# Kernel optimization log

Measured on AMD Instinct MI355X. Metric: run time of the kernel, lower is better.

The kernel has to match this reference:

```python
import jax, jax.numpy as jnp
import numpy as np

N = 50000      # nodes
E = 800000     # edges (avg degree 16)
DIN = 128
H = 128
DOUT = 64


def setup_inputs() -> dict:
    key = jax.random.key(0)
    ks = jax.random.split(key, 8)
    x = jax.random.normal(ks[0], (N, DIN), dtype=jnp.float32)
    edge_index = jax.random.randint(ks[1], (2, E), 0, N, dtype=jnp.int32)
    def glorot(k, fi, fo):
        return jax.random.normal(k, (fi, fo), dtype=jnp.float32) * (1.0 / np.sqrt(fi))
    return {
        "x": x,
        "edge_index": edge_index,
        "W1": glorot(ks[2], DIN, H), "b1": jnp.zeros((H,), jnp.float32),
        "W2": glorot(ks[3], H, H),   "b2": jnp.zeros((H,), jnp.float32),
        "W3": glorot(ks[4], H, DOUT),"b3": jnp.zeros((DOUT,), jnp.float32),
    }


def reference(x, edge_index, W1, b1, W2, b2, W3, b3):
    n = x.shape[0]
    # GCNConv: add self-loops, symmetric degree normalization D^-1/2 (A+I) D^-1/2
    loop = jnp.arange(n, dtype=edge_index.dtype)
    src = jnp.concatenate([edge_index[0], loop])  # [E+N]
    dst = jnp.concatenate([edge_index[1], loop])
    deg = jax.ops.segment_sum(jnp.ones(src.shape, x.dtype), dst, num_segments=n)
    dinv = jnp.where(deg > 0, jax.lax.rsqrt(deg), 0.0)
    norm = dinv[src] * dinv[dst]  # [E+N]

    def conv(h, W, b):
        h = h @ W                                   # [N, out]
        msg = h[src] * norm[:, None]                # gather + scale
        return jax.ops.segment_sum(msg, dst, num_segments=n) + b

    # gelu after every layer except the last (forward breaks before act)
    h = jax.nn.gelu(conv(x, W1, b1), approximate=False)
    h = jax.nn.gelu(conv(h, W2, b2), approximate=False)
    return conv(h, W3, b3)
```

## Files before the change

kernel.cpp:

```cpp
#include <hip/hip_runtime.h>
#include <math.h>

#define NDIN 128
#define NHID 128
#define NDOUT 64

typedef _Float16 half2_t __attribute__((ext_vector_type(2)));
typedef _Float16 half4_t __attribute__((ext_vector_type(4)));
typedef _Float16 half8_t __attribute__((ext_vector_type(8)));
typedef float    float4v __attribute__((ext_vector_type(4)));

__device__ __forceinline__ float gelu_exact(float x) {
    return 0.5f * x * (1.0f + erff(x * 0.70710678118654752f));
}


__global__ void count_kernel(const int* __restrict__ dst, int* __restrict__ count, int E) {
    int e = blockIdx.x * blockDim.x + threadIdx.x;
    if (e < E) atomicAdd(&count[dst[e]], 1);
}

__global__ __launch_bounds__(256) void reduce_blocks_kernel(
    const int* __restrict__ count, int* __restrict__ blocksum, int n) {
    __shared__ int s[256];
    int i = blockIdx.x * 256 + threadIdx.x;
    s[threadIdx.x] = (i < n) ? count[i] : 0;
    __syncthreads();
    for (int off = 128; off > 0; off >>= 1) {
        if (threadIdx.x < off) s[threadIdx.x] += s[threadIdx.x + off];
        __syncthreads();
    }
    if (threadIdx.x == 0) blocksum[blockIdx.x] = s[0];
}

__global__ __launch_bounds__(256) void scan_partials_kernel(
    const int* __restrict__ blocksum, int* __restrict__ blockoff,
    int* __restrict__ rowptr, int nb, int n) {
    __shared__ int s[256];
    int t = threadIdx.x;
    int v = (t < nb) ? blocksum[t] : 0;
    s[t] = v;
    __syncthreads();
    for (int off = 1; off < 256; off <<= 1) {
        int u = (t >= off) ? s[t - off] : 0;
        __syncthreads();
        s[t] += u;
        __syncthreads();
    }
    if (t < nb) blockoff[t] = s[t] - v;
    if (t == 255) rowptr[n] = s[255];
}

__global__ __launch_bounds__(256) void scan_blocks_kernel(
    const int* __restrict__ count, const int* __restrict__ blockoff,
    int* __restrict__ rowptr, float* __restrict__ dinv, int n) {
    __shared__ int s[256];
    int i = blockIdx.x * 256 + threadIdx.x;
    int v = (i < n) ? count[i] : 0;
    s[threadIdx.x] = v;
    __syncthreads();
    for (int off = 1; off < 256; off <<= 1) {
        int u = (threadIdx.x >= off) ? s[threadIdx.x - off] : 0;
        __syncthreads();
        s[threadIdx.x] += u;
        __syncthreads();
    }
    if (i < n) {
        rowptr[i] = blockoff[blockIdx.x] + s[threadIdx.x] - v;
        dinv[i] = rsqrtf((float)(v + 1));
    }
}

__global__ void fill_kernel(const int* __restrict__ src, const int* __restrict__ dst,
                            const float* __restrict__ dinv, const int* __restrict__ rowptr,
                            int* __restrict__ count, int2* __restrict__ adj, int E) {
    int e = blockIdx.x * blockDim.x + threadIdx.x;
    if (e >= E) return;
    int s = src[e], d = dst[e];
    int slot = atomicSub(&count[d], 1) - 1;
    int p = rowptr[d] + slot;
    adj[p] = make_int2(s, __float_as_int(dinv[s] * dinv[d]));
}

__global__ __launch_bounds__(256) void wtrans_kernel(
    const float* __restrict__ W, _Float16* __restrict__ Wt, int K, int N) {
    __shared__ float tile[32][33];
    int tx = threadIdx.x & 31, ty = threadIdx.x >> 5;
    for (int i = 0; i < 32; i += 8) {
        int k = blockIdx.y * 32 + ty + i, n = blockIdx.x * 32 + tx;
        tile[ty + i][tx] = (k < K && n < N) ? W[(size_t)k * N + n] : 0.f;
    }
    __syncthreads();
    for (int i = 0; i < 32; i += 8) {
        int n = blockIdx.x * 32 + ty + i, k = blockIdx.y * 32 + tx;
        if (n < N && k < K) Wt[(size_t)n * K + k] = (_Float16)tile[tx][ty + i];
    }
}


template <int BN, bool AF16>
__global__ __launch_bounds__(256) void gemm_mfma(
    const void* __restrict__ Aptr, const _Float16* __restrict__ Bt,
    _Float16* __restrict__ T, int M) {
    __shared__ _Float16 lds_a[64][136];
    __shared__ _Float16 lds_bt[BN][136];
    const int K = 128;
    int tid = threadIdx.x;
    int bm = blockIdx.x * 64;
    int wave = tid >> 6, lane = tid & 63;
    int m = lane & 15, quad = lane >> 4;

    if (AF16) {
        const _Float16* A = (const _Float16*)Aptr;
#pragma unroll
        for (int j = 0; j < 4; j++) {
            int c = tid + j * 256;
            int r = c >> 4, col = (c & 15) << 3;
            int grow = bm + r;
            uint4 v = make_uint4(0, 0, 0, 0);
            if (grow < M) v = *(const uint4*)(A + (size_t)grow * K + col);
            *(uint4*)&lds_a[r][col] = v;
        }
    } else {
        const float* A = (const float*)Aptr;
#pragma unroll
        for (int j = 0; j < 8; j++) {
            int c = tid + j * 256;
            int r = c >> 5, col = (c & 31) << 2;
            int grow = bm + r;
            float4 v = make_float4(0.f, 0.f, 0.f, 0.f);
            if (grow < M) v = *(const float4*)(A + (size_t)grow * K + col);
            half4_t h;
            h[0] = (_Float16)v.x; h[1] = (_Float16)v.y;
            h[2] = (_Float16)v.z; h[3] = (_Float16)v.w;
            *(half4_t*)&lds_a[r][col] = h;
        }
    }
    {
        const int chunks = BN * K / 8;
        for (int c = tid; c < chunks; c += 256) {
            int r = c >> 4, col = (c & 15) << 3;
            *(uint4*)&lds_bt[r][col] = *(const uint4*)(Bt + (size_t)r * K + col);
        }
    }
    __syncthreads();

    const int NT = BN / 16;
    float4v acc[NT];
#pragma unroll
    for (int nt = 0; nt < NT; nt++) acc[nt] = (float4v){0.f, 0.f, 0.f, 0.f};

    int arow = (wave << 4) + m;
#pragma unroll
    for (int kc = 0; kc < K; kc += 32) {
        half8_t a = *(const half8_t*)&lds_a[arow][kc + quad * 8];
#pragma unroll
        for (int nt = 0; nt < NT; nt++) {
            half8_t b = *(const half8_t*)&lds_bt[nt * 16 + m][kc + quad * 8];
            acc[nt] = __builtin_amdgcn_mfma_f32_16x16x32_f16(a, b, acc[nt], 0, 0, 0);
        }
    }
#pragma unroll
    for (int nt = 0; nt < NT; nt++) {
#pragma unroll
        for (int r = 0; r < 4; r++) {
            int grow = bm + (wave << 4) + (quad << 2) + r;
            if (grow < M) T[(size_t)grow * BN + nt * 16 + m] = (_Float16)acc[nt][r];
        }
    }
}


template <int F, bool DOGELU, bool OUTF16>
__global__ __launch_bounds__(256) void agg_kernel(
    const _Float16* __restrict__ t, const int* __restrict__ rowptr,
    const int2* __restrict__ adj, const float* __restrict__ dinv,
    const float* __restrict__ bias, void* __restrict__ outp, int n) {
    int node = (int)((blockIdx.x * blockDim.x + threadIdx.x) >> 6);
    int lane = threadIdx.x & 63;
    if (node >= n) return;

    float wself = dinv[node];
    wself *= wself;
    int beg = rowptr[node];
    int end = rowptr[node + 1];

    if (F == 128) {
        const half2_t* t2 = (const half2_t*)t;
        half2_t v = t2[(size_t)node * 64 + lane];
        float accx = wself * (float)v[0], accy = wself * (float)v[1];
        for (int e0 = beg; e0 < end; e0 += 64) {
            int rem = end - e0;
            int j = 0; float w = 0.f;
            if (lane < rem) {
                int2 ed = adj[e0 + lane];
                j = ed.x; w = __int_as_float(ed.y);
            }
            int cnt = rem < 64 ? rem : 64;
            for (int c = 0; c < cnt; c += 16) {
#pragma unroll
                for (int i = 0; i < 16; i++) {
                    int jj = __builtin_amdgcn_readlane(j, c + i);
                    float ww = __int_as_float(
                        __builtin_amdgcn_readlane(__float_as_int(w), c + i));
                    half2_t u = t2[(size_t)jj * 64 + lane];
                    accx += ww * (float)u[0];
                    accy += ww * (float)u[1];
                }
            }
        }
        float2 b = ((const float2*)bias)[lane];
        accx += b.x; accy += b.y;
        if (DOGELU) { accx = gelu_exact(accx); accy = gelu_exact(accy); }
        if (OUTF16) {
            half2_t o; o[0] = (_Float16)accx; o[1] = (_Float16)accy;
            ((half2_t*)outp)[(size_t)node * 64 + lane] = o;
        } else {
            float2 o; o.x = accx; o.y = accy;
            ((float2*)outp)[(size_t)node * 64 + lane] = o;
        }
    } else {
        float acc = wself * (float)t[(size_t)node * 64 + lane];
        for (int e0 = beg; e0 < end; e0 += 64) {
            int rem = end - e0;
            int j = 0; float w = 0.f;
            if (lane < rem) {
                int2 ed = adj[e0 + lane];
                j = ed.x; w = __int_as_float(ed.y);
            }
            int cnt = rem < 64 ? rem : 64;
            for (int c = 0; c < cnt; c += 16) {
#pragma unroll
                for (int i = 0; i < 16; i++) {
                    int jj = __builtin_amdgcn_readlane(j, c + i);
                    float ww = __int_as_float(
                        __builtin_amdgcn_readlane(__float_as_int(w), c + i));
                    acc += ww * (float)t[(size_t)jj * 64 + lane];
                }
            }
        }
        acc += bias[lane];
        if (DOGELU) acc = gelu_exact(acc);
        if (OUTF16) ((_Float16*)outp)[(size_t)node * 64 + lane] = (_Float16)acc;
        else        ((float*)outp)[(size_t)node * 64 + lane] = acc;
    }
}


extern "C" void kernel_launch(void* const* d_in, const int* in_sizes, int n_in,
                              void* d_out, int out_size, void* d_ws, size_t ws_size,
                              hipStream_t stream) {
    const float* x  = (const float*)d_in[0];
    const int* edge = (const int*)d_in[1];
    const float* W1 = (const float*)d_in[2];
    const float* b1 = (const float*)d_in[3];
    const float* W2 = (const float*)d_in[4];
    const float* b2 = (const float*)d_in[5];
    const float* W3 = (const float*)d_in[6];
    const float* b3 = (const float*)d_in[7];
    float* out = (float*)d_out;

    const int N = in_sizes[0] / NDIN;
    const int E = in_sizes[1] / 2;
    const int* src = edge;
    const int* dst = edge + E;
    const int NB = (N + 255) / 256;

    char* p = (char*)d_ws;
    auto alloc = [&](size_t bytes) {
        char* q = p;
        p += (bytes + 255) & ~(size_t)255;
        return q;
    };
    int*       count    = (int*)alloc((size_t)N * 4);
    int*       rowptr   = (int*)alloc((size_t)(N + 1) * 4);
    int*       blocksum = (int*)alloc((size_t)NB * 4);
    int*       blockoff = (int*)alloc((size_t)NB * 4);
    float*     dinv     = (float*)alloc((size_t)N * 4);
    int2*      adj      = (int2*)alloc((size_t)E * 8);
    _Float16*  W1t      = (_Float16*)alloc((size_t)NHID * NDIN * 2);
    _Float16*  W2t      = (_Float16*)alloc((size_t)NHID * NHID * 2);
    _Float16*  W3t      = (_Float16*)alloc((size_t)NDOUT * NHID * 2);
    _Float16*  tbuf     = (_Float16*)alloc((size_t)N * NHID * 2);
    _Float16*  hbuf     = (_Float16*)alloc((size_t)N * NHID * 2);

    hipMemsetAsync(count, 0, (size_t)N * 4, stream);

    count_kernel<<<(E + 255) / 256, 256, 0, stream>>>(dst, count, E);
    reduce_blocks_kernel<<<NB, 256, 0, stream>>>(count, blocksum, N);
    scan_partials_kernel<<<1, 256, 0, stream>>>(blocksum, blockoff, rowptr, NB, N);
    scan_blocks_kernel<<<NB, 256, 0, stream>>>(count, blockoff, rowptr, dinv, N);
    fill_kernel<<<(E + 255) / 256, 256, 0, stream>>>(src, dst, dinv, rowptr, count,
                                                     adj, E);
    wtrans_kernel<<<dim3(NHID / 32, NDIN / 32), 256, 0, stream>>>(W1, W1t, NDIN, NHID);
    wtrans_kernel<<<dim3(NHID / 32, NHID / 32), 256, 0, stream>>>(W2, W2t, NHID, NHID);
    wtrans_kernel<<<dim3(NDOUT / 32, NHID / 32), 256, 0, stream>>>(W3, W3t, NHID, NDOUT);

    dim3 blk(256);
    int mtiles = (N + 63) / 64;
    int agg_blocks = (N + 3) / 4;

    gemm_mfma<128, false><<<mtiles, blk, 0, stream>>>(x, W1t, tbuf, N);
    agg_kernel<128, true, true><<<agg_blocks, blk, 0, stream>>>(tbuf, rowptr, adj,
                                                                dinv, b1, hbuf, N);
    gemm_mfma<128, true><<<mtiles, blk, 0, stream>>>(hbuf, W2t, tbuf, N);
    agg_kernel<128, true, true><<<agg_blocks, blk, 0, stream>>>(tbuf, rowptr, adj,
                                                                dinv, b2, hbuf, N);
    gemm_mfma<64, true><<<mtiles, blk, 0, stream>>>(hbuf, W3t, tbuf, N);
    agg_kernel<64, false, false><<<agg_blocks, blk, 0, stream>>>(tbuf, rowptr, adj,
                                                                 dinv, b3, out, N);
}
```

Measured before the change: 292.7 us.

## Merge preprocessing launches and vectorize aggregation with 16-byte gathers

Folds the memset and three weight transposes into one prep kernel. The block reduce and partial scan become a single kernel using a last-block-done atomic, and the edge fill is co-launched with the first GEMM. The aggregation kernel now has lane groups each handle a different neighbor with 8-wide half loads, followed by a cross-group shuffle reduction. The goal is to cut launch overhead and issue fewer, wider gather loads, at the cost of extra shuffle reductions and idle lanes during the epilogue.

```diff
diff --git a/kernel.cpp b/kernel.cpp
--- a/kernel.cpp
+++ b/kernel.cpp
@@ -15,30 +15,71 @@
 }
 
 
+__device__ void wtrans_tile(const float* __restrict__ W, _Float16* __restrict__ Wt,
+                            int K, int N, int bx, int by) {
+    __shared__ float tile[32][33];
+    int tx = threadIdx.x & 31, ty = threadIdx.x >> 5;
+    for (int i = 0; i < 32; i += 8) {
+        int k = by * 32 + ty + i, nn = bx * 32 + tx;
+        tile[ty + i][tx] = (k < K && nn < N) ? W[(size_t)k * N + nn] : 0.f;
+    }
+    __syncthreads();
+    for (int i = 0; i < 32; i += 8) {
+        int nn = bx * 32 + ty + i, k = by * 32 + tx;
+        if (nn < N && k < K) Wt[(size_t)nn * K + k] = (_Float16)tile[tx][ty + i];
+    }
+}
+
+__global__ __launch_bounds__(256) void prep0_kernel(
+    const float* __restrict__ W1, _Float16* __restrict__ W1t,
+    const float* __restrict__ W2, _Float16* __restrict__ W2t,
+    const float* __restrict__ W3, _Float16* __restrict__ W3t,
+    int* __restrict__ count, int* __restrict__ done, int n) {
+    int b = blockIdx.x;
+    if (b < 16) {
+        wtrans_tile(W1, W1t, NDIN, NHID, b & 3, b >> 2);
+    } else if (b < 32) {
+        wtrans_tile(W2, W2t, NHID, NHID, (b - 16) & 3, (b - 16) >> 2);
+    } else if (b < 40) {
+        wtrans_tile(W3, W3t, NHID, NDOUT, (b - 32) & 1, (b - 32) >> 1);
+    } else {
+        int z = b - 40;
+        int i = z * 256 + threadIdx.x;
+        if (i < n) count[i] = 0;
+        if (z == 0 && threadIdx.x == 0) *done = 0;
+    }
+}
+
+
 __global__ void count_kernel(const int* __restrict__ dst, int* __restrict__ count, int E) {
     int e = blockIdx.x * blockDim.x + threadIdx.x;
     if (e < E) atomicAdd(&count[dst[e]], 1);
 }
 
-__global__ __launch_bounds__(256) void reduce_blocks_kernel(
-    const int* __restrict__ count, int* __restrict__ blocksum, int n) {
+
+__global__ __launch_bounds__(256) void reduce_scanp_kernel(
+    const int* __restrict__ count, int* __restrict__ blocksum, int* __restrict__ blockoff,
+    int* __restrict__ rowptr, int* __restrict__ done, int nb, int n) {
     __shared__ int s[256];
-    int i = blockIdx.x * 256 + threadIdx.x;
-    s[threadIdx.x] = (i < n) ? count[i] : 0;
+    __shared__ int islast;
+    int t = threadIdx.x;
+    int i = blockIdx.x * 256 + t;
+    s[t] = (i < n) ? count[i] : 0;
     __syncthreads();
     for (int off = 128; off > 0; off >>= 1) {
-        if (threadIdx.x < off) s[threadIdx.x] += s[threadIdx.x + off];
-        __syncthreads();
-    }
-    if (threadIdx.x == 0) blocksum[blockIdx.x] = s[0];
-}
-
-__global__ __launch_bounds__(256) void scan_partials_kernel(
-    const int* __restrict__ blocksum, int* __restrict__ blockoff,
-    int* __restrict__ rowptr, int nb, int n) {
-    __shared__ int s[256];
-    int t = threadIdx.x;
-    int v = (t < nb) ? blocksum[t] : 0;
+        if (t < off) s[t] += s[t + off];
+        __syncthreads();
+    }
+    if (t == 0) {
+        atomicExch(&blocksum[blockIdx.x], s[0]);
+        __threadfence();
+        int old = atomicAdd(done, 1);
+        islast = (old == nb - 1) ? 1 : 0;
+    }
+    __syncthreads();
+    if (!islast) return;
+    __threadfence();
+    int v = (t < nb) ? atomicAdd(&blocksum[t], 0) : 0;
     s[t] = v;
     __syncthreads();
     for (int off = 1; off < 256; off <<= 1) {
@@ -50,6 +91,7 @@
     if (t < nb) blockoff[t] = s[t] - v;
     if (t == 255) rowptr[n] = s[255];
 }
+
 
 __global__ __launch_bounds__(256) void scan_blocks_kernel(
     const int* __restrict__ count, const int* __restrict__ blockoff,
@@ -71,42 +113,15 @@
     }
 }
 
-__global__ void fill_kernel(const int* __restrict__ src, const int* __restrict__ dst,
-                            const float* __restrict__ dinv, const int* __restrict__ rowptr,
-                            int* __restrict__ count, int2* __restrict__ adj, int E) {
-    int e = blockIdx.x * blockDim.x + threadIdx.x;
-    if (e >= E) return;
-    int s = src[e], d = dst[e];
-    int slot = atomicSub(&count[d], 1) - 1;
-    int p = rowptr[d] + slot;
-    adj[p] = make_int2(s, __float_as_int(dinv[s] * dinv[d]));
-}
-
-__global__ __launch_bounds__(256) void wtrans_kernel(
-    const float* __restrict__ W, _Float16* __restrict__ Wt, int K, int N) {
-    __shared__ float tile[32][33];
-    int tx = threadIdx.x & 31, ty = threadIdx.x >> 5;
-    for (int i = 0; i < 32; i += 8) {
-        int k = blockIdx.y * 32 + ty + i, n = blockIdx.x * 32 + tx;
-        tile[ty + i][tx] = (k < K && n < N) ? W[(size_t)k * N + n] : 0.f;
-    }
-    __syncthreads();
-    for (int i = 0; i < 32; i += 8) {
-        int n = blockIdx.x * 32 + ty + i, k = blockIdx.y * 32 + tx;
-        if (n < N && k < K) Wt[(size_t)n * K + k] = (_Float16)tile[tx][ty + i];
-    }
-}
-
 
 template <int BN, bool AF16>
-__global__ __launch_bounds__(256) void gemm_mfma(
-    const void* __restrict__ Aptr, const _Float16* __restrict__ Bt,
-    _Float16* __restrict__ T, int M) {
+__device__ void gemm_body(const void* __restrict__ Aptr, const _Float16* __restrict__ Bt,
+                          _Float16* __restrict__ T, int M, int blk) {
     __shared__ _Float16 lds_a[64][136];
     __shared__ _Float16 lds_bt[BN][136];
     const int K = 128;
     int tid = threadIdx.x;
-    int bm = blockIdx.x * 64;
+    int bm = blk * 64;
     int wave = tid >> 6, lane = tid & 63;
     int m = lane & 15, quad = lane >> 4;
 
@@ -170,79 +185,107 @@
     }
 }
 
+template <int BN, bool AF16>
+__global__ __launch_bounds__(256) void gemm_mfma(
+    const void* __restrict__ Aptr, const _Float16* __restrict__ Bt,
+    _Float16* __restrict__ T, int M) {
+    gemm_body<BN, AF16>(Aptr, Bt, T, M, blockIdx.x);
+}
+
+
+__global__ __launch_bounds__(256) void fill_gemm1_kernel(
+    const int* __restrict__ src, const int* __restrict__ dst,
+    const float* __restrict__ dinv, const int* __restrict__ rowptr,
+    int* __restrict__ count, int2* __restrict__ adj, int E,
+    const float* __restrict__ x, const _Float16* __restrict__ W1t,
+    _Float16* __restrict__ T, int M, int gemmBlocks) {
+    int b = blockIdx.x;
+    if (b < gemmBlocks) {
+        gemm_body<128, false>(x, W1t, T, M, b);
+        return;
+    }
+    int e = (b - gemmBlocks) * 256 + threadIdx.x;
+    if (e >= E) return;
+    int s = src[e], d = dst[e];
+    int slot = atomicSub(&count[d], 1) - 1;
+    int p = rowptr[d] + slot;
+    adj[p] = make_int2(s, __float_as_int(dinv[s] * dinv[d]));
+}
+
 
 template <int F, bool DOGELU, bool OUTF16>
 __global__ __launch_bounds__(256) void agg_kernel(
     const _Float16* __restrict__ t, const int* __restrict__ rowptr,
     const int2* __restrict__ adj, const float* __restrict__ dinv,
     const float* __restrict__ bias, void* __restrict__ outp, int n) {
+    constexpr int LPG = F / 8;
+    constexpr int NG  = 64 / LPG;
     int node = (int)((blockIdx.x * blockDim.x + threadIdx.x) >> 6);
     int lane = threadIdx.x & 63;
     if (node >= n) return;
 
+    int g = lane / LPG;
+    int lsub = lane % LPG;
+
+    float acc[8];
+#pragma unroll
+    for (int f = 0; f < 8; f++) acc[f] = 0.f;
+
     float wself = dinv[node];
     wself *= wself;
+    if (g == 0) {
+        half8_t u = *(const half8_t*)(t + (size_t)node * F + lsub * 8);
+#pragma unroll
+        for (int f = 0; f < 8; f++) acc[f] = wself * (float)u[f];
+    }
+
     int beg = rowptr[node];
     int end = rowptr[node + 1];
-
-    if (F == 128) {
-        const half2_t* t2 = (const half2_t*)t;
-        half2_t v = t2[(size_t)node * 64 + lane];
-        float accx = wself * (float)v[0], accy = wself * (float)v[1];
-        for (int e0 = beg; e0 < end; e0 += 64) {
-            int rem = end - e0;
-            int j = 0; float w = 0.f;
-            if (lane < rem) {
-                int2 ed = adj[e0 + lane];
-                j = ed.x; w = __int_as_float(ed.y);
-            }
-            int cnt = rem < 64 ? rem : 64;
-            for (int c = 0; c < cnt; c += 16) {
-#pragma unroll
-                for (int i = 0; i < 16; i++) {
-                    int jj = __builtin_amdgcn_readlane(j, c + i);
-                    float ww = __int_as_float(
-                        __builtin_amdgcn_readlane(__float_as_int(w), c + i));
-                    half2_t u = t2[(size_t)jj * 64 + lane];
-                    accx += ww * (float)u[0];
-                    accy += ww * (float)u[1];
-                }
-            }
-        }
-        float2 b = ((const float2*)bias)[lane];
-        accx += b.x; accy += b.y;
-        if (DOGELU) { accx = gelu_exact(accx); accy = gelu_exact(accy); }
+    for (int e0 = beg; e0 < end; e0 += 64) {
+        int rem = end - e0;
+        int j = 0; float w = 0.f;
+        if (lane < rem) {
+            int2 ed = adj[e0 + lane];
+            j = ed.x; w = __int_as_float(ed.y);
+        }
+        int cnt = rem < 64 ? rem : 64;
+        int iters = (cnt + NG - 1) / NG;
+#pragma unroll 4
+        for (int it = 0; it < iters; it++) {
+            int srcl = it * NG + g;
+            int jj = __shfl(j, srcl);
+            float ww = __shfl(w, srcl);
+            half8_t u = *(const half8_t*)(t + (size_t)jj * F + lsub * 8);
+#pragma unroll
+            for (int f = 0; f < 8; f++) acc[f] += ww * (float)u[f];
+        }
+    }
+#pragma unroll
+    for (int off = LPG; off < 64; off <<= 1)
+#pragma unroll
+        for (int f = 0; f < 8; f++) acc[f] += __shfl_xor(acc[f], off);
+
+    if (g == 0) {
+        float4 b0 = *(const float4*)(bias + lsub * 8);
+        float4 b1 = *(const float4*)(bias + lsub * 8 + 4);
+        acc[0] += b0.x; acc[1] += b0.y; acc[2] += b0.z; acc[3] += b0.w;
+        acc[4] += b1.x; acc[5] += b1.y; acc[6] += b1.z; acc[7] += b1.w;
+        if (DOGELU) {
+#pragma unroll
+            for (int f = 0; f < 8; f++) acc[f] = gelu_exact(acc[f]);
+        }
         if (OUTF16) {
-            half2_t o; o[0] = (_Float16)accx; o[1] = (_Float16)accy;
-            ((half2_t*)outp)[(size_t)node * 64 + lane] = o;
+            half8_t o;
+#pragma unroll
+            for (int f = 0; f < 8; f++) o[f] = (_Float16)acc[f];
+            *(half8_t*)((_Float16*)outp + (size_t)node * F + lsub * 8) = o;
         } else {
-            float2 o; o.x = accx; o.y = accy;
-            ((float2*)outp)[(size_t)node * 64 + lane] = o;
-        }
-    } else {
-        float acc = wself * (float)t[(size_t)node * 64 + lane];
-        for (int e0 = beg; e0 < end; e0 += 64) {
-            int rem = end - e0;
-            int j = 0; float w = 0.f;
-            if (lane < rem) {
-                int2 ed = adj[e0 + lane];
-                j = ed.x; w = __int_as_float(ed.y);
-            }
-            int cnt = rem < 64 ? rem : 64;
-            for (int c = 0; c < cnt; c += 16) {
-#pragma unroll
-                for (int i = 0; i < 16; i++) {
-                    int jj = __builtin_amdgcn_readlane(j, c + i);
-                    float ww = __int_as_float(
-                        __builtin_amdgcn_readlane(__float_as_int(w), c + i));
-                    acc += ww * (float)t[(size_t)jj * 64 + lane];
-                }
-            }
-        }
-        acc += bias[lane];
-        if (DOGELU) acc = gelu_exact(acc);
-        if (OUTF16) ((_Float16*)outp)[(size_t)node * 64 + lane] = (_Float16)acc;
-        else        ((float*)outp)[(size_t)node * 64 + lane] = acc;
+            float* op = (float*)outp + (size_t)node * F + lsub * 8;
+            float4 o0 = make_float4(acc[0], acc[1], acc[2], acc[3]);
+            float4 o1 = make_float4(acc[4], acc[5], acc[6], acc[7]);
+            *(float4*)op = o0;
+            *(float4*)(op + 4) = o1;
+        }
     }
 }
 
@@ -276,6 +319,7 @@
     int*       rowptr   = (int*)alloc((size_t)(N + 1) * 4);
     int*       blocksum = (int*)alloc((size_t)NB * 4);
     int*       blockoff = (int*)alloc((size_t)NB * 4);
+    int*       done     = (int*)alloc(256);
     float*     dinv     = (float*)alloc((size_t)N * 4);
     int2*      adj      = (int2*)alloc((size_t)E * 8);
     _Float16*  W1t      = (_Float16*)alloc((size_t)NHID * NDIN * 2);
@@ -284,23 +328,18 @@
     _Float16*  tbuf     = (_Float16*)alloc((size_t)N * NHID * 2);
     _Float16*  hbuf     = (_Float16*)alloc((size_t)N * NHID * 2);
 
-    hipMemsetAsync(count, 0, (size_t)N * 4, stream);
-
-    count_kernel<<<(E + 255) / 256, 256, 0, stream>>>(dst, count, E);
-    reduce_blocks_kernel<<<NB, 256, 0, stream>>>(count, blocksum, N);
-    scan_partials_kernel<<<1, 256, 0, stream>>>(blocksum, blockoff, rowptr, NB, N);
-    scan_blocks_kernel<<<NB, 256, 0, stream>>>(count, blockoff, rowptr, dinv, N);
-    fill_kernel<<<(E + 255) / 256, 256, 0, stream>>>(src, dst, dinv, rowptr, count,
-                                                     adj, E);
-    wtrans_kernel<<<dim3(NHID / 32, NDIN / 32), 256, 0, stream>>>(W1, W1t, NDIN, NHID);
-    wtrans_kernel<<<dim3(NHID / 32, NHID / 32), 256, 0, stream>>>(W2, W2t, NHID, NHID);
-    wtrans_kernel<<<dim3(NDOUT / 32, NHID / 32), 256, 0, stream>>>(W3, W3t, NHID, NDOUT);
-
     dim3 blk(256);
     int mtiles = (N + 63) / 64;
+    int eblocks = (E + 255) / 256;
     int agg_blocks = (N + 3) / 4;
 
-    gemm_mfma<128, false><<<mtiles, blk, 0, stream>>>(x, W1t, tbuf, N);
+    prep0_kernel<<<40 + NB, blk, 0, stream>>>(W1, W1t, W2, W2t, W3, W3t, count, done, N);
+    count_kernel<<<eblocks, blk, 0, stream>>>(dst, count, E);
+    reduce_scanp_kernel<<<NB, blk, 0, stream>>>(count, blocksum, blockoff, rowptr,
+                                                done, NB, N);
+    scan_blocks_kernel<<<NB, blk, 0, stream>>>(count, blockoff, rowptr, dinv, N);
+    fill_gemm1_kernel<<<mtiles + eblocks, blk, 0, stream>>>(
+        src, dst, dinv, rowptr, count, adj, E, x, W1t, tbuf, N, mtiles);
     agg_kernel<128, true, true><<<agg_blocks, blk, 0, stream>>>(tbuf, rowptr, adj,
                                                                 dinv, b1, hbuf, N);
     gemm_mfma<128, true><<<mtiles, blk, 0, stream>>>(hbuf, W2t, tbuf, N);
```

Result: slower. 304.0 us (+3.9%).
